# Kernel tuning notes

Measured on AMD Instinct MI355X. Metric: run time of the kernel, lower is better.

Reference implementation:

```python
import jax, jax.numpy as jnp
import numpy as np
import math

NUM_HEADS = 16
ATTN_WIDTH = 256


def setup_inputs() -> dict:
    key = jax.random.key(0)
    ks = jax.random.split(key, 5)
    B, S, C, H = 2, 2048, 1024, 1024
    scale = 0.02
    return {
        "x": jax.random.normal(ks[0], (B, S, C), dtype=jnp.float32),
        "Wq": jax.random.normal(ks[1], (C, H), dtype=jnp.float32) * scale,
        "Wk": jax.random.normal(ks[2], (C, H), dtype=jnp.float32) * scale,
        "Wv": jax.random.normal(ks[3], (C, H), dtype=jnp.float32) * scale,
        "Wo": jax.random.normal(ks[4], (H, C), dtype=jnp.float32) * scale,
    }


def reference(x, Wq, Wk, Wv, Wo):
    B, S, C = x.shape
    H = NUM_HEADS
    dh = Wq.shape[1] // H  # head dim; Q.size(-1) in torch code

    def split_heads(t):
        # [B, S, H*dh] -> [B, H, S, dh]
        return t.reshape(B, S, H, dh).transpose(0, 2, 1, 3)

    q = split_heads(x @ Wq)
    k = split_heads(x @ Wk)
    v = split_heads(x @ Wv)

    scores = jnp.einsum("bhqd,bhkd->bhqk", q, k) / math.sqrt(dh)
    # exp-shift (first 'softmax-like' step, unnormalized)
    scores = jnp.exp(scores - jnp.max(scores, axis=-1, keepdims=True))
    # banded mask: tril(attn_width//2 - 1).triu(-(attn_width//2))
    i = jnp.arange(S)[:, None]
    j = jnp.arange(S)[None, :]
    d = j - i
    half = ATTN_WIDTH // 2
    mask = (d <= half - 1) & (d >= -half)
    scores = jnp.where(mask, scores, 0.0)
    # second softmax over the masked exp-scores (zeros contribute exp(0)=1)
    weights = jax.nn.softmax(scores, axis=-1)

    out = jnp.einsum("bhqk,bhkd->bhqd", weights, v)  # [B, H, S, dh]
    out = out.transpose(0, 2, 1, 3).reshape(B, S, H * dh)
    return out @ Wo
```

## Files before the change

kernel.cpp:

```cpp
#include <hip/hip_runtime.h>
#include <math.h>

typedef __bf16 bf16_t;
typedef bf16_t bf16x8 __attribute__((ext_vector_type(8)));
typedef bf16_t bf16x4 __attribute__((ext_vector_type(4)));
typedef float f32x4 __attribute__((ext_vector_type(4)));

constexpr int S_ = 2048;
constexpr float SCALE = 0.125f;

#define MFMA_B16(a, b, c) __builtin_amdgcn_mfma_f32_16x16x32_bf16(a, b, c, 0, 0, 0)

typedef __attribute__((address_space(1))) const void* as1_cvp;
typedef __attribute__((address_space(3))) void* as3_vp;

__device__ __forceinline__ void gl2lds16(const void* g, void* l)
{
    __builtin_amdgcn_global_load_lds((as1_cvp)g, (as3_vp)l, 16, 0, 0);
}

__global__ __launch_bounds__(256) void prep(const float* __restrict__ x,
                                            const float* __restrict__ Wq,
                                            const float* __restrict__ Wk,
                                            const float* __restrict__ Wv,
                                            const float* __restrict__ Wo,
                                            bf16_t* __restrict__ xb,
                                            bf16_t* __restrict__ Wqt,
                                            bf16_t* __restrict__ Wkt,
                                            bf16_t* __restrict__ Wvt,
                                            bf16_t* __restrict__ Wot,
                                            float* __restrict__ vsp)
{
    __shared__ float T[64][65];
    const int blk = blockIdx.x;
    const int tid = threadIdx.x;
    if (blk < 1024) {
#pragma unroll
        for (int u = 0; u < 4; ++u) {
            const int g = blk * 1024 + u * 256 + tid;
            const float4 v = ((const float4*)x)[g];
            bf16x4 o;
            o[0] = (bf16_t)v.x; o[1] = (bf16_t)v.y;
            o[2] = (bf16_t)v.z; o[3] = (bf16_t)v.w;
            *(bf16x4*)&xb[(size_t)g * 4] = o;
        }
    } else if (blk < 2048) {
        const int rem = blk - 1024;
        const int wsel = rem >> 8, t = rem & 255;
        const float* src = (wsel == 0) ? Wq : (wsel == 1) ? Wk : (wsel == 2) ? Wv : Wo;
        bf16_t* dst = (wsel == 0) ? Wqt : (wsel == 1) ? Wkt : (wsel == 2) ? Wvt : Wot;
        const int k0 = (t >> 4) * 64, n0 = (t & 15) * 64;
        const int rr = tid >> 4, c4 = (tid & 15) * 4;
#pragma unroll
        for (int u = 0; u < 4; ++u) {
            const float4 v = *(const float4*)&src[(size_t)(k0 + u * 16 + rr) * 1024 + n0 + c4];
            T[u * 16 + rr][c4 + 0] = v.x; T[u * 16 + rr][c4 + 1] = v.y;
            T[u * 16 + rr][c4 + 2] = v.z; T[u * 16 + rr][c4 + 3] = v.w;
        }
        __syncthreads();
#pragma unroll
        for (int u = 0; u < 4; ++u) {
            bf16x4 o;
#pragma unroll
            for (int e = 0; e < 4; ++e) o[e] = (bf16_t)T[c4 + e][u * 16 + rr];
            *(bf16x4*)&dst[(size_t)(n0 + u * 16 + rr) * 1024 + k0 + c4] = o;
        }
    } else {
#pragma unroll
        for (int u = 0; u < 8; ++u) vsp[u * 256 + tid] = 0.f;
    }
}

template <int MODE>
__device__ __forceinline__ void mfma_gemm_body(const bf16_t* __restrict__ A,
                                               const bf16_t* __restrict__ Bt,
                                               void* __restrict__ dst,
                                               float* __restrict__ vsum_out,
                                               int m0, int n0)
{
    __shared__ bf16_t As[4096];
    __shared__ bf16_t Bs[4096];

    const int tid = threadIdx.x;
    const int lane = tid & 63, wid = tid >> 6;
    const int l15 = lane & 15, quad = lane >> 4;
    const int wm = (wid & 1) * 64, wn = (wid >> 1) * 64;

    const int srow = wid * 32 + (lane >> 2);
    const int scg8 = (lane & 3) * 8;
    const bf16_t* Ag0 = A  + (size_t)(m0 + srow) * 1024 + scg8;
    const bf16_t* Ag1 = A  + (size_t)(m0 + srow + 16) * 1024 + scg8;
    const bf16_t* Bg0 = Bt + (size_t)(n0 + srow) * 1024 + scg8;
    const bf16_t* Bg1 = Bt + (size_t)(n0 + srow + 16) * 1024 + scg8;
    bf16_t* Al0 = As + (wid * 2 + 0) * 512;
    bf16_t* Al1 = As + (wid * 2 + 1) * 512;
    bf16_t* Bl0 = Bs + (wid * 2 + 0) * 512;
    bf16_t* Bl1 = Bs + (wid * 2 + 1) * 512;

    f32x4 acc[4][4];
#pragma unroll
    for (int i = 0; i < 4; ++i)
#pragma unroll
        for (int j = 0; j < 4; ++j) acc[i][j] = (f32x4){0.f, 0.f, 0.f, 0.f};

    for (int k0 = 0; k0 < 1024; k0 += 32) {
        __syncthreads();
        gl2lds16(Ag0 + k0, Al0);
        gl2lds16(Ag1 + k0, Al1);
        gl2lds16(Bg0 + k0, Bl0);
        gl2lds16(Bg1 + k0, Bl1);
        __syncthreads();

        bf16x8 af[4], bfr[4];
#pragma unroll
        for (int mt = 0; mt < 4; ++mt)
            af[mt] = *(const bf16x8*)&As[(wm + mt * 16 + l15) * 32 + quad * 8];
#pragma unroll
        for (int nt = 0; nt < 4; ++nt)
            bfr[nt] = *(const bf16x8*)&Bs[(wn + nt * 16 + l15) * 32 + quad * 8];
#pragma unroll
        for (int mt = 0; mt < 4; ++mt)
#pragma unroll
            for (int nt = 0; nt < 4; ++nt)
                acc[mt][nt] = MFMA_B16(bfr[nt], af[mt], acc[mt][nt]);
    }

#pragma unroll
    for (int mt = 0; mt < 4; ++mt) {
        const int m = m0 + wm + mt * 16 + l15;
#pragma unroll
        for (int nt = 0; nt < 4; ++nt) {
            const int nb = n0 + wn + nt * 16 + quad * 4;
            if (MODE == 0) {
                *(f32x4*)&((float*)dst)[(size_t)m * 1024 + nb] = acc[mt][nt];
            } else {
                const int bb = m >> 11, s = m & 2047;
                const int hh = nb >> 6, d = nb & 63;
                bf16x4 o;
#pragma unroll
                for (int u = 0; u < 4; ++u) o[u] = (bf16_t)acc[mt][nt][u];
                *(bf16x4*)&((bf16_t*)dst)[((size_t)(bb * 16 + hh) * 2048 + s) * 64 + d] = o;
            }
        }
    }

    if (MODE == 1 && vsum_out != nullptr) {
        const int bb = m0 >> 11;
#pragma unroll
        for (int nt = 0; nt < 4; ++nt) {
            f32x4 p = acc[0][nt];
#pragma unroll
            for (int mt = 1; mt < 4; ++mt) {
                p[0] += acc[mt][nt][0]; p[1] += acc[mt][nt][1];
                p[2] += acc[mt][nt][2]; p[3] += acc[mt][nt][3];
            }
#pragma unroll
            for (int st = 1; st < 16; st <<= 1) {
                p[0] += __shfl_xor(p[0], st);
                p[1] += __shfl_xor(p[1], st);
                p[2] += __shfl_xor(p[2], st);
                p[3] += __shfl_xor(p[3], st);
            }
            if (l15 == 0) {
                const int nI = n0 + wn + nt * 16 + quad * 4;
                float* vp = &vsum_out[(bb * 16 + (nI >> 6)) * 64 + (nI & 63)];
                atomicAdd(vp + 0, p[0]);
                atomicAdd(vp + 1, p[1]);
                atomicAdd(vp + 2, p[2]);
                atomicAdd(vp + 3, p[3]);
            }
        }
    }
}

__global__ __launch_bounds__(256) void gemm_qkv_mfma(const bf16_t* __restrict__ xb,
                                                     const bf16_t* __restrict__ Wqt,
                                                     const bf16_t* __restrict__ Wkt,
                                                     const bf16_t* __restrict__ Wvt,
                                                     bf16_t* Qh, bf16_t* Kh, bf16_t* Vh,
                                                     float* vsp)
{
    const bf16_t* Bt = (blockIdx.z == 0) ? Wqt : (blockIdx.z == 1) ? Wkt : Wvt;
    bf16_t* dst = (blockIdx.z == 0) ? Qh : (blockIdx.z == 1) ? Kh : Vh;
    float* vs = (blockIdx.z == 2) ? vsp : nullptr;
    mfma_gemm_body<1>(xb, Bt, dst, vs, blockIdx.y * 128, blockIdx.x * 128);
}

__global__ __launch_bounds__(256) void gemm_out_mfma(const bf16_t* __restrict__ attn,
                                                     const bf16_t* __restrict__ Wot,
                                                     float* __restrict__ out)
{
    mfma_gemm_body<0>(attn, Wot, out, nullptr, blockIdx.y * 128, blockIdx.x * 128);
}

__global__ __launch_bounds__(256, 2) void attn_fused(const bf16_t* __restrict__ Qh,
                                                     const bf16_t* __restrict__ Kh,
                                                     const bf16_t* __restrict__ Vh,
                                                     const float* __restrict__ vsp,
                                                     bf16_t* __restrict__ attn)
{
    __shared__ bf16_t Qs[8192];
    __shared__ bf16_t pool[17920];
    __shared__ float msh[4][8][16];
    __shared__ float zsh[4][32];

    bf16_t* Ks2 = pool;
    bf16_t* Vt  = pool + 4096;
    bf16_t* Ws  = pool + 8704;

    const int tid = threadIdx.x;
    const int lane = tid & 63, wid = tid >> 6;
    const int l15 = lane & 15, quad = lane >> 4;

    const int f = blockIdx.x;
    const int seq = f >> 3;
    const int bh = (f & 7) + 8 * (seq >> 4);
    const int i0 = (seq & 15) * 128;
    const int b = bh >> 4, h = bh & 15;
    const bf16_t* Qb = Qh + (size_t)bh * 131072;
    const bf16_t* Kb = Kh + (size_t)bh * 131072;
    const bf16_t* Vb = Vh + (size_t)bh * 131072;

#pragma unroll
    for (int c = 0; c < 4; ++c) {
        const int g = wid * 4 + c;
        const int half = g >> 3;
        const int row = (g & 7) * 16 + (lane >> 2);
        gl2lds16(Qb + (size_t)(i0 + row) * 64 + half * 32 + (lane & 3) * 8,
                 Qs + g * 512);
    }
    __syncthreads();

    bf16x8 af[8][2];
#pragma unroll
    for (int mt = 0; mt < 8; ++mt)
#pragma unroll
        for (int ks = 0; ks < 2; ++ks)
            af[mt][ks] = *(const bf16x8*)&Qs[ks * 4096 + (mt * 16 + l15) * 32 + quad * 8];

    float rmax[8];
#pragma unroll
    for (int mt = 0; mt < 8; ++mt) rmax[mt] = -3.0e38f;

    for (int jc = 0; jc < 8; ++jc) {
        __syncthreads();
#pragma unroll
        for (int c = 0; c < 8; ++c) {
            const int g = wid * 8 + c;
            const int half = g >> 4;
            const int row = (g & 15) * 16 + (lane >> 2);
            gl2lds16(Kb + (size_t)(jc * 256 + row) * 64 + half * 32 + (lane & 3) * 8,
                     pool + g * 512);
        }
        __syncthreads();
#pragma unroll
        for (int ntl = 0; ntl < 4; ++ntl) {
            const int jt = wid * 4 + ntl;
            const bf16x8 b0 = *(const bf16x8*)&pool[(jt * 16 + l15) * 32 + quad * 8];
            const bf16x8 b1 = *(const bf16x8*)&pool[8192 + (jt * 16 + l15) * 32 + quad * 8];
#pragma unroll
            for (int mt = 0; mt < 8; ++mt) {
                f32x4 t = (f32x4){0.f, 0.f, 0.f, 0.f};
                t = MFMA_B16(b0, af[mt][0], t);
                t = MFMA_B16(b1, af[mt][1], t);
                rmax[mt] = fmaxf(rmax[mt], fmaxf(fmaxf(t[0], t[1]), fmaxf(t[2], t[3])));
            }
        }
    }
#pragma unroll
    for (int mt = 0; mt < 8; ++mt) {
        float v = rmax[mt];
        v = fmaxf(v, __shfl_xor(v, 16));
        v = fmaxf(v, __shfl_xor(v, 32));
        if (quad == 0) msh[wid][mt][l15] = v;
    }
    __syncthreads();

    float mreg[2][4];
#pragma unroll
    for (int t = 0; t < 2; ++t)
#pragma unroll
        for (int r = 0; r < 4; ++r) {
            const int mt = wid * 2 + t;
            const int il = quad * 4 + r;
            mreg[t][r] = SCALE * fmaxf(fmaxf(msh[0][mt][il], msh[1][mt][il]),
                                       fmaxf(msh[2][mt][il], msh[3][mt][il]));
        }

    f32x4 vsd4[4];
#pragma unroll
    for (int dt = 0; dt < 4; ++dt)
        vsd4[dt] = *(const f32x4*)&vsp[bh * 64 + dt * 16 + quad * 4];

    f32x4 accO[2][4];
#pragma unroll
    for (int t = 0; t < 2; ++t)
#pragma unroll
        for (int dt = 0; dt < 4; ++dt) accO[t][dt] = (f32x4){0.f, 0.f, 0.f, 0.f};
    float zp[2][4] = {{0.f, 0.f, 0.f, 0.f}, {0.f, 0.f, 0.f, 0.f}};

    for (int cb = 0; cb < 6; ++cb) {
        const int jb = i0 - 128 + cb * 64;
        if (jb < 0 || jb >= S_) continue;

        __syncthreads();
#pragma unroll
        for (int c = 0; c < 2; ++c) {
            const int g = wid * 2 + c;
            const int half = g >> 2;
            const int row = (g & 3) * 16 + (lane >> 2);
            gl2lds16(Kb + (size_t)(jb + row) * 64 + half * 32 + (lane & 3) * 8,
                     Ks2 + g * 512);
        }
        {
            const bf16x8 v0 = *(const bf16x8*)&Vb[(size_t)(jb + lane) * 64 + wid * 16];
            const bf16x8 v1 = *(const bf16x8*)&Vb[(size_t)(jb + lane) * 64 + wid * 16 + 8];
#pragma unroll
            for (int e = 0; e < 8; ++e) {
                Vt[(wid * 16 + e) * 72 + lane] = v0[e];
                Vt[(wid * 16 + 8 + e) * 72 + lane] = v1[e];
            }
        }
        __syncthreads();

#pragma unroll
        for (int t = 0; t < 2; ++t) {
            const int mt = wid * 2 + t;
#pragma unroll
            for (int jt4 = 0; jt4 < 4; ++jt4) {
                const bf16x8 k0 = *(const bf16x8*)&Ks2[(jt4 * 16 + l15) * 32 + quad * 8];
                const bf16x8 k1 = *(const bf16x8*)&Ks2[2048 + (jt4 * 16 + l15) * 32 + quad * 8];
                f32x4 sc = (f32x4){0.f, 0.f, 0.f, 0.f};
                sc = MFMA_B16(af[mt][0], k0, sc);
                sc = MFMA_B16(af[mt][1], k1, sc);
#pragma unroll
                for (int r = 0; r < 4; ++r) {
                    const int ig = i0 + mt * 16 + quad * 4 + r;
                    const int jg = jb + jt4 * 16 + l15;
                    const int dd = jg - ig;
                    const bool ok = (dd >= -128) && (dd <= 127);
                    const float e1 = __expf(sc[r] * SCALE - mreg[t][r]);
                    const float wv = ok ? (__expf(e1) - 1.0f) : 0.0f;
                    const bf16_t wb = (bf16_t)wv;
                    zp[t][r] += (float)wb;
                    Ws[(mt * 16 + quad * 4 + r) * 72 + jt4 * 16 + l15] = wb;
                }
            }
        }
        __syncthreads();

#pragma unroll
        for (int ks = 0; ks < 2; ++ks) {
            bf16x8 bv[4];
#pragma unroll
            for (int dt = 0; dt < 4; ++dt)
                bv[dt] = *(const bf16x8*)&Vt[(dt * 16 + l15) * 72 + ks * 32 + quad * 8];
#pragma unroll
            for (int t = 0; t < 2; ++t) {
                const int mt = wid * 2 + t;
                const bf16x8 aw = *(const bf16x8*)&Ws[(mt * 16 + l15) * 72 + ks * 32 + quad * 8];
#pragma unroll
                for (int dt = 0; dt < 4; ++dt)
                    accO[t][dt] = MFMA_B16(bv[dt], aw, accO[t][dt]);
            }
        }
    }

#pragma unroll
    for (int t = 0; t < 2; ++t)
#pragma unroll
        for (int r = 0; r < 4; ++r) {
            float z = zp[t][r];
            z += __shfl_xor(z, 1);
            z += __shfl_xor(z, 2);
            z += __shfl_xor(z, 4);
            z += __shfl_xor(z, 8);
            if (l15 == 0) zsh[wid][t * 16 + quad * 4 + r] = z + (float)S_;
        }
    __syncthreads();

#pragma unroll
    for (int t = 0; t < 2; ++t) {
        const float rz = 1.0f / zsh[wid][t * 16 + l15];
        const int irow = i0 + (wid * 2 + t) * 16 + l15;
#pragma unroll
        for (int dt = 0; dt < 4; ++dt) {
            bf16x4 o;
#pragma unroll
            for (int r = 0; r < 4; ++r)
                o[r] = (bf16_t)((accO[t][dt][r] + vsd4[dt][r]) * rz);
            *(bf16x4*)&attn[(size_t)(b * S_ + irow) * 1024 + h * 64 + dt * 16 + quad * 4] = o;
        }
    }
}

extern "C" void kernel_launch(void* const* d_in, const int* in_sizes, int n_in,
                              void* d_out, int out_size, void* d_ws, size_t ws_size,
                              hipStream_t stream)
{
    const float* x  = (const float*)d_in[0];
    const float* Wq = (const float*)d_in[1];
    const float* Wk = (const float*)d_in[2];
    const float* Wv = (const float*)d_in[3];
    const float* Wo = (const float*)d_in[4];
    float* out = (float*)d_out;

    char* ws = (char*)d_ws;
    bf16_t* xb   = (bf16_t*)(ws + 0);
    bf16_t* Wqt  = (bf16_t*)(ws + 8388608);
    bf16_t* Wkt  = (bf16_t*)(ws + 10485760);
    bf16_t* Wvt  = (bf16_t*)(ws + 12582912);
    bf16_t* Wot  = (bf16_t*)(ws + 14680064);
    bf16_t* Qh   = (bf16_t*)(ws + 16777216);
    bf16_t* Kh   = (bf16_t*)(ws + 25165824);
    bf16_t* Vh   = (bf16_t*)(ws + 33554432);
    bf16_t* attn = (bf16_t*)(ws + 41943040);
    float*  vsp  = (float*)(ws + 50331648);

    prep<<<2049, 256, 0, stream>>>(x, Wq, Wk, Wv, Wo, xb, Wqt, Wkt, Wvt, Wot, vsp);
    gemm_qkv_mfma<<<dim3(8, 32, 3), 256, 0, stream>>>(xb, Wqt, Wkt, Wvt, Qh, Kh, Vh, vsp);
    attn_fused<<<512, 256, 0, stream>>>(Qh, Kh, Vh, vsp, attn);
    gemm_out_mfma<<<dim3(8, 32), 256, 0, stream>>>(attn, Wot, out);
}
```

Measured before the change: 189.2 us.

## Double-buffer LDS loads in GEMM and attention max pass, raise attn occupancy

The GEMM K-loop now double-buffers its LDS tiles, issuing global-to-LDS loads for the next K slice before computing on the current one, with a single wait and barrier per iteration. The attention row-max pass processes 128-key chunks with ping-pong buffers, prefetching the next chunk while computing. Q staging reuses the shared pool and zsh aliases msh, which reduces LDS use so attention can target 4 blocks per CU. The aim is to hide global memory latency and raise occupancy, at the cost of more LDS in the GEMM and tighter register limits in attention.

```diff
diff --git a/kernel.cpp b/kernel.cpp
--- a/kernel.cpp
+++ b/kernel.cpp
@@ -10,6 +10,10 @@
 constexpr float SCALE = 0.125f;
 
 #define MFMA_B16(a, b, c) __builtin_amdgcn_mfma_f32_16x16x32_bf16(a, b, c, 0, 0, 0)
+
+#define WAIT_VM0()   __builtin_amdgcn_s_waitcnt(0x0F70)
+#define WAIT_LGKM0() __builtin_amdgcn_s_waitcnt(0xC07F)
+#define BARRIER()    __builtin_amdgcn_s_barrier()
 
 typedef __attribute__((address_space(1))) const void* as1_cvp;
 typedef __attribute__((address_space(3))) void* as3_vp;
@@ -78,8 +82,8 @@
                                                float* __restrict__ vsum_out,
                                                int m0, int n0)
 {
-    __shared__ bf16_t As[4096];
-    __shared__ bf16_t Bs[4096];
+    __shared__ bf16_t As[8192];
+    __shared__ bf16_t Bs[8192];
 
     const int tid = threadIdx.x;
     const int lane = tid & 63, wid = tid >> 6;
@@ -92,10 +96,6 @@
     const bf16_t* Ag1 = A  + (size_t)(m0 + srow + 16) * 1024 + scg8;
     const bf16_t* Bg0 = Bt + (size_t)(n0 + srow) * 1024 + scg8;
     const bf16_t* Bg1 = Bt + (size_t)(n0 + srow + 16) * 1024 + scg8;
-    bf16_t* Al0 = As + (wid * 2 + 0) * 512;
-    bf16_t* Al1 = As + (wid * 2 + 1) * 512;
-    bf16_t* Bl0 = Bs + (wid * 2 + 0) * 512;
-    bf16_t* Bl1 = Bs + (wid * 2 + 1) * 512;
 
     f32x4 acc[4][4];
 #pragma unroll
@@ -103,21 +103,29 @@
 #pragma unroll
         for (int j = 0; j < 4; ++j) acc[i][j] = (f32x4){0.f, 0.f, 0.f, 0.f};
 
-    for (int k0 = 0; k0 < 1024; k0 += 32) {
-        __syncthreads();
-        gl2lds16(Ag0 + k0, Al0);
-        gl2lds16(Ag1 + k0, Al1);
-        gl2lds16(Bg0 + k0, Bl0);
-        gl2lds16(Bg1 + k0, Bl1);
-        __syncthreads();
-
+    gl2lds16(Ag0, As + (wid * 2 + 0) * 512);
+    gl2lds16(Ag1, As + (wid * 2 + 1) * 512);
+    gl2lds16(Bg0, Bs + (wid * 2 + 0) * 512);
+    gl2lds16(Bg1, Bs + (wid * 2 + 1) * 512);
+
+    for (int it = 0; it < 32; ++it) {
+        WAIT_VM0();
+        BARRIER();
+        const int cur = it & 1, nxt = cur ^ 1;
+        if (it + 1 < 32) {
+            const int k0 = (it + 1) * 32;
+            gl2lds16(Ag0 + k0, As + nxt * 4096 + (wid * 2 + 0) * 512);
+            gl2lds16(Ag1 + k0, As + nxt * 4096 + (wid * 2 + 1) * 512);
+            gl2lds16(Bg0 + k0, Bs + nxt * 4096 + (wid * 2 + 0) * 512);
+            gl2lds16(Bg1 + k0, Bs + nxt * 4096 + (wid * 2 + 1) * 512);
+        }
         bf16x8 af[4], bfr[4];
 #pragma unroll
         for (int mt = 0; mt < 4; ++mt)
-            af[mt] = *(const bf16x8*)&As[(wm + mt * 16 + l15) * 32 + quad * 8];
+            af[mt] = *(const bf16x8*)&As[cur * 4096 + (wm + mt * 16 + l15) * 32 + quad * 8];
 #pragma unroll
         for (int nt = 0; nt < 4; ++nt)
-            bfr[nt] = *(const bf16x8*)&Bs[(wn + nt * 16 + l15) * 32 + quad * 8];
+            bfr[nt] = *(const bf16x8*)&Bs[cur * 4096 + (wn + nt * 16 + l15) * 32 + quad * 8];
 #pragma unroll
         for (int mt = 0; mt < 4; ++mt)
 #pragma unroll
@@ -193,20 +201,19 @@
     mfma_gemm_body<0>(attn, Wot, out, nullptr, blockIdx.y * 128, blockIdx.x * 128);
 }
 
-__global__ __launch_bounds__(256, 2) void attn_fused(const bf16_t* __restrict__ Qh,
+__global__ __launch_bounds__(256, 4) void attn_fused(const bf16_t* __restrict__ Qh,
                                                      const bf16_t* __restrict__ Kh,
                                                      const bf16_t* __restrict__ Vh,
                                                      const float* __restrict__ vsp,
                                                      bf16_t* __restrict__ attn)
 {
-    __shared__ bf16_t Qs[8192];
     __shared__ bf16_t pool[17920];
     __shared__ float msh[4][8][16];
-    __shared__ float zsh[4][32];
 
     bf16_t* Ks2 = pool;
     bf16_t* Vt  = pool + 4096;
     bf16_t* Ws  = pool + 8704;
+    float (*zsh)[32] = (float(*)[32])msh;
 
     const int tid = threadIdx.x;
     const int lane = tid & 63, wid = tid >> 6;
@@ -227,37 +234,45 @@
         const int half = g >> 3;
         const int row = (g & 7) * 16 + (lane >> 2);
         gl2lds16(Qb + (size_t)(i0 + row) * 64 + half * 32 + (lane & 3) * 8,
-                 Qs + g * 512);
-    }
-    __syncthreads();
+                 pool + g * 512);
+        gl2lds16(Kb + (size_t)row * 64 + half * 32 + (lane & 3) * 8,
+                 pool + 8192 + g * 512);
+    }
+    WAIT_VM0();
+    BARRIER();
 
     bf16x8 af[8][2];
 #pragma unroll
     for (int mt = 0; mt < 8; ++mt)
 #pragma unroll
         for (int ks = 0; ks < 2; ++ks)
-            af[mt][ks] = *(const bf16x8*)&Qs[ks * 4096 + (mt * 16 + l15) * 32 + quad * 8];
+            af[mt][ks] = *(const bf16x8*)&pool[ks * 4096 + (mt * 16 + l15) * 32 + quad * 8];
+    WAIT_LGKM0();
 
     float rmax[8];
 #pragma unroll
     for (int mt = 0; mt < 8; ++mt) rmax[mt] = -3.0e38f;
 
-    for (int jc = 0; jc < 8; ++jc) {
-        __syncthreads();
-#pragma unroll
-        for (int c = 0; c < 8; ++c) {
-            const int g = wid * 8 + c;
-            const int half = g >> 4;
-            const int row = (g & 15) * 16 + (lane >> 2);
-            gl2lds16(Kb + (size_t)(jc * 256 + row) * 64 + half * 32 + (lane & 3) * 8,
-                     pool + g * 512);
-        }
-        __syncthreads();
-#pragma unroll
-        for (int ntl = 0; ntl < 4; ++ntl) {
-            const int jt = wid * 4 + ntl;
-            const bf16x8 b0 = *(const bf16x8*)&pool[(jt * 16 + l15) * 32 + quad * 8];
-            const bf16x8 b1 = *(const bf16x8*)&pool[8192 + (jt * 16 + l15) * 32 + quad * 8];
+    for (int jc = 0; jc < 16; ++jc) {
+        if (jc) WAIT_VM0();
+        BARRIER();
+        if (jc + 1 < 16) {
+            bf16_t* nb = pool + (jc & 1) * 8192;
+#pragma unroll
+            for (int c = 0; c < 4; ++c) {
+                const int g = wid * 4 + c;
+                const int half = g >> 3;
+                const int row = (g & 7) * 16 + (lane >> 2);
+                gl2lds16(Kb + (size_t)((jc + 1) * 128 + row) * 64 + half * 32 + (lane & 3) * 8,
+                         nb + g * 512);
+            }
+        }
+        const bf16_t* cb = pool + (((jc + 1) & 1)) * 8192;
+#pragma unroll
+        for (int ntl = 0; ntl < 2; ++ntl) {
+            const int jt = wid * 2 + ntl;
+            const bf16x8 b0 = *(const bf16x8*)&cb[(jt * 16 + l15) * 32 + quad * 8];
+            const bf16x8 b1 = *(const bf16x8*)&cb[4096 + (jt * 16 + l15) * 32 + quad * 8];
 #pragma unroll
             for (int mt = 0; mt < 8; ++mt) {
                 f32x4 t = (f32x4){0.f, 0.f, 0.f, 0.f};
@@ -299,8 +314,8 @@
         for (int dt = 0; dt < 4; ++dt) accO[t][dt] = (f32x4){0.f, 0.f, 0.f, 0.f};
     float zp[2][4] = {{0.f, 0.f, 0.f, 0.f}, {0.f, 0.f, 0.f, 0.f}};
 
-    for (int cb = 0; cb < 6; ++cb) {
-        const int jb = i0 - 128 + cb * 64;
+    for (int cb2 = 0; cb2 < 6; ++cb2) {
+        const int jb = i0 - 128 + cb2 * 64;
         if (jb < 0 || jb >= S_) continue;
 
         __syncthreads();
```

Result: slower. 208.9 us (+10.4%).
